# Kernel optimization log

Measured on AMD Instinct MI355X. Metric: run time of the kernel, lower is better.

## Reference

```python
import jax, jax.numpy as jnp
import numpy as np

N, L, H, DH = 4, 1024, 16, 64
D = H * DH  # 1024
DFF = 4 * D
NEG_INF = jnp.float32(-1e30)  # used via actual -inf per torch masked_fill


def layer_norm(x, g, b, eps=1e-5):
    mu = jnp.mean(x, axis=-1, keepdims=True)
    var = jnp.mean(jnp.square(x - mu), axis=-1, keepdims=True)
    return (x - mu) * jax.lax.rsqrt(var + eps) * g + b


def mha(q_in, k_in, Wq, Wk, Wv, mask, padding_mask):
    # q_in: (N,Lq,D), k_in: (N,Lk,D); Linear weights (D,D), out = x @ W.T
    n, Lq, _ = q_in.shape
    Lk = k_in.shape[1]
    q = jnp.einsum('nld,od->nlo', q_in, Wq).reshape(n, Lq, H, DH)
    k = jnp.einsum('nld,od->nlo', k_in, Wk).reshape(n, Lk, H, DH)
    v = jnp.einsum('nld,od->nlo', k_in, Wv).reshape(n, Lk, H, DH)
    # per-sample scaling = sqrt(#non-padded keys)
    scaling = jnp.sqrt(jnp.sum(~padding_mask, axis=-1).astype(q.dtype))  # (N,)
    score = jnp.einsum('nqhd,nkhd->nhqk', q, k) / scaling[:, None, None, None]
    if mask is not None:
        score = jnp.where(mask[None, None, :, :], -jnp.inf, score)
    score = jnp.where(padding_mask[:, None, None, :], -jnp.inf, score)
    p = jax.nn.softmax(score, axis=-1)
    out = jnp.einsum('nhqk,nkhd->nqhd', p, v).reshape(n, Lq, D)
    return out


def setup_inputs() -> dict:
    key = jax.random.key(0)
    ks = jax.random.split(key, 16)
    s = 0.02
    inp = {
        'encoded': jax.random.normal(ks[0], (N, L, D), jnp.float32),
        'Y': jax.random.normal(ks[1], (N, L, D), jnp.float32),
        # causal mask: True above diagonal -> attention set to -inf
        'mask': ~jnp.tril(jnp.ones((L, L), dtype=bool)),
        # suffix padding with varied per-sample lengths (all >= 1)
        'padding_mask': jnp.arange(L)[None, :] >= jnp.array([L, 3 * L // 4, L // 2, 7 * L // 8])[:, None],
        # masked self-attention projections
        'Wq1': jax.random.normal(ks[2], (D, D), jnp.float32) * s,
        'Wk1': jax.random.normal(ks[3], (D, D), jnp.float32) * s,
        'Wv1': jax.random.normal(ks[4], (D, D), jnp.float32) * s,
        'g1': jnp.ones((D,), jnp.float32), 'b1': jnp.zeros((D,), jnp.float32),
        # cross-attention projections
        'Wq2': jax.random.normal(ks[5], (D, D), jnp.float32) * s,
        'Wk2': jax.random.normal(ks[6], (D, D), jnp.float32) * s,
        'Wv2': jax.random.normal(ks[7], (D, D), jnp.float32) * s,
        'g2': jnp.ones((D,), jnp.float32), 'b2': jnp.zeros((D,), jnp.float32),
        # FFN
        'We': jax.random.normal(ks[8], (DFF, D), jnp.float32) * s,
        'be': jnp.zeros((DFF,), jnp.float32),
        'Wc': jax.random.normal(ks[9], (D, DFF), jnp.float32) * s,
        'bc': jnp.zeros((D,), jnp.float32),
        'g3': jnp.ones((D,), jnp.float32), 'b3': jnp.zeros((D,), jnp.float32),
    }
    return inp


def reference(encoded, Y, mask, padding_mask,
              Wq1, Wk1, Wv1, g1, b1,
              Wq2, Wk2, Wv2, g2, b2,
              We, be, Wc, bc, g3, b3):
    # masked self-attention + residual + LN (dropout=0 -> identity)
    res = Y
    a = mha(Y, Y, Wq1, Wk1, Wv1, mask, padding_mask)
    Y = layer_norm(a + res, g1, b1)
    # cross-attention (no causal mask) + residual + LN
    res = Y
    a = mha(Y, encoded, Wq2, Wk2, Wv2, None, padding_mask)
    Y = layer_norm(a + res, g2, b2)
    # FFN + residual + LN
    res = Y
    h = jax.nn.relu(jnp.einsum('nld,fd->nlf', Y, We) + be)
    h = jnp.einsum('nlf,df->nld', h, Wc) + bc
    Y = layer_norm(h + res, g3, b3)
    return Y
```

## Files before the change

### kernel.cpp

```cpp
#include <hip/hip_runtime.h>
#include <stdint.h>

#define NB 4
#define LS 1024
#define HH 16
#define DHD 64
#define DM 1024
#define DF 4096
#define QKS 2048

typedef unsigned short u16;
typedef __attribute__((ext_vector_type(4))) float f32x4;
typedef __attribute__((ext_vector_type(8))) __bf16 bf16x8;
typedef __attribute__((ext_vector_type(8))) unsigned short u16x8;

__device__ __forceinline__ u16 f2bf(float f) {
  union { float f; uint32_t u; } v; v.f = f;
  uint32_t u = v.u;
  return (u16)((u + 0x7fffu + ((u >> 16) & 1u)) >> 16);
}

__device__ __forceinline__ bf16x8 ldb8(const u16* p) {
  u16x8 r = *(const u16x8*)p;
  return __builtin_bit_cast(bf16x8, r);
}

__device__ __forceinline__ void gload_lds16(const u16* g, u16* l) {
  __builtin_amdgcn_global_load_lds((const __attribute__((address_space(1))) void*)g,
                                   (__attribute__((address_space(3))) void*)l,
                                   16, 0, 0);
}

#define WAITV10() asm volatile("s_waitcnt vmcnt(10)" ::: "memory")
#define BARRIER()                      \
  do {                                 \
    asm volatile("" ::: "memory");     \
    __builtin_amdgcn_s_barrier();      \
    asm volatile("" ::: "memory");     \
  } while (0)

__global__ void prep_kernel(const uint32_t* __restrict__ pm, int* lens, float* iscl) {
  __shared__ int flagByte;
  __shared__ int red[256];
  int tid = threadIdx.x;
  if (tid == 0) flagByte = 0;
  __syncthreads();
  int f = 0;
  for (int w = tid; w < (NB * LS) / 4; w += 256) {
    uint32_t u = pm[w];
    if (u != 0u && u != 1u && u != 0x3f800000u) f = 1;
  }
  if (f) atomicOr(&flagByte, 1);
  __syncthreads();
  int isByte = flagByte;
  for (int n = 0; n < NB; n++) {
    int c = 0;
    if (isByte) {
      const uint8_t* pb = (const uint8_t*)pm;
      for (int l = tid; l < LS; l += 256) c += (pb[n * LS + l] == 0) ? 1 : 0;
    } else {
      for (int l = tid; l < LS; l += 256) c += (pm[n * LS + l] == 0) ? 1 : 0;
    }
    red[tid] = c;
    __syncthreads();
    for (int s = 128; s > 0; s >>= 1) {
      if (tid < s) red[tid] += red[tid + s];
      __syncthreads();
    }
    if (tid == 0) { lens[n] = red[0]; iscl[n] = 1.0f / sqrtf((float)red[0]); }
    __syncthreads();
  }
}

__global__ void cvt_all(const float* s0, u16* d0, const float* s1, u16* d1,
                        const float* s2, u16* d2, const float* s3, u16* d3,
                        const float* s4, u16* d4, const float* s5, u16* d5,
                        const float* s6, u16* d6, const float* s7, u16* d7,
                        const float* s8, u16* d8, const float* s9, u16* d9) {
  const int total = 5767168;
  int i = blockIdx.x * 256 + threadIdx.x;
  for (; i < total; i += gridDim.x * 256) {
    const float* s; u16* d; int j;
    if (i < 1048576)      { s = s0; d = d0; j = i; }
    else if (i < 2097152) { s = s1; d = d1; j = i - 1048576; }
    else if (i < 2359296) { s = s2; d = d2; j = i - 2097152; }
    else if (i < 2621440) { s = s3; d = d3; j = i - 2359296; }
    else if (i < 2883584) { s = s4; d = d4; j = i - 2621440; }
    else if (i < 3145728) { s = s5; d = d5; j = i - 2883584; }
    else if (i < 3407872) { s = s6; d = d6; j = i - 3145728; }
    else if (i < 3670016) { s = s7; d = d7; j = i - 3407872; }
    else if (i < 4718592) { s = s8; d = d8; j = i - 3670016; }
    else                  { s = s9; d = d9; j = i - 4718592; }
    float4 fv = ((const float4*)s)[j];
    ushort4 o;
    o.x = f2bf(fv.x); o.y = f2bf(fv.y); o.z = f2bf(fv.z); o.w = f2bf(fv.w);
    ((ushort4*)d)[j] = o;
  }
}

template <int MODE>
__global__ __launch_bounds__(512, 2) void gemm8(
    const u16* __restrict__ P0, const u16* __restrict__ P1,
    const u16* __restrict__ PW, const float* __restrict__ bias,
    void* __restrict__ O0, void* __restrict__ O1,
    void* __restrict__ O2, void* __restrict__ O3) {
  extern __shared__ u16 lds[];
  constexpr int NT = 16;
  const int bm = blockIdx.x;
  const int tid = threadIdx.x;
  const int wid = tid >> 6, lane = tid & 63;
  const int lrow = lane & 15, lgrp = lane >> 4;
  const int wm = wid >> 2, wn = wid & 3;

  const u16* Asrc; const u16* Bsrc; int lda, ldb;
  if constexpr (MODE == 0) {
    Asrc = P0 + (size_t)bm * 256 * DM; lda = DM;
    Bsrc = PW + (size_t)blockIdx.y * 256 * DM; ldb = DM;
  } else if constexpr (MODE == 1) {
    const int z = blockIdx.z;
    Asrc = P0 + (size_t)bm * 256 * DF + z * 1024; lda = DF;
    Bsrc = PW + (size_t)blockIdx.y * 256 * DF + z * 1024; ldb = DF;
  } else {
    const int bnt = blockIdx.y;
    Asrc = (bnt < 12 ? P0 : P1) + (size_t)bm * 256 * DM; lda = DM;
    const int wrow = (bnt < 12) ? bnt * 256 : 4096 + (bnt - 12) * 256;
    Bsrc = PW + (size_t)wrow * DM; ldb = DM;
  }

  int srow[2], skk[2];
#pragma unroll
  for (int i = 0; i < 2; i++) {
    const int c = (i * 8 + wid) * 64 + lane;
    const int pair = c >> 3;
    const int ue = ((c & 7) * 8) ^ ((pair & 7) << 3);
    srow[i] = pair * 2 + (ue >> 5);
    skk[i] = ue & 31;
  }
  const int dslot0 = wid * 512;
  const int dslot1 = (8 + wid) * 512;

  f32x4 acc[2][4][4] = {};

  auto STAGE_A = [&](int kt, int buf, int kh) {
    const int ks = kt < NT ? kt : NT - 1;
    gload_lds16(Asrc + (size_t)srow[0] * lda + ks * 64 + kh * 32 + skk[0],
                lds + buf * 16384 + kh * 8192 + dslot0);
    gload_lds16(Asrc + (size_t)srow[1] * lda + ks * 64 + kh * 32 + skk[1],
                lds + buf * 16384 + kh * 8192 + dslot1);
  };
  auto STAGE_B = [&](int kt, int buf, int kh) {
    const int ks = kt < NT ? kt : NT - 1;
    gload_lds16(Bsrc + (size_t)srow[0] * ldb + ks * 64 + kh * 32 + skk[0],
                lds + 32768 + buf * 16384 + kh * 8192 + dslot0);
    gload_lds16(Bsrc + (size_t)srow[1] * ldb + ks * 64 + kh * 32 + skk[1],
                lds + 32768 + buf * 16384 + kh * 8192 + dslot1);
  };
  auto LDA = [&](int buf, int kh, int mh, bf16x8* a) {
#pragma unroll
    for (int m = 0; m < 4; m++) {
      const int row = wm * 128 + mh * 64 + m * 16 + lrow;
      const int idx = buf * 16384 + kh * 8192 + (row >> 1) * 64 +
                      ((((row & 1) << 5) + (lgrp << 3)) ^ (((row >> 1) & 7) << 3));
      a[m] = ldb8(lds + idx);
    }
  };
  auto LDB = [&](int buf, int kh, bf16x8* b) {
#pragma unroll
    for (int nn = 0; nn < 4; nn++) {
      const int row = wn * 64 + nn * 16 + lrow;
      const int idx = 32768 + buf * 16384 + kh * 8192 + (row >> 1) * 64 +
                      ((((row & 1) << 5) + (lgrp << 3)) ^ (((row >> 1) & 7) << 3));
      b[nn] = ldb8(lds + idx);
    }
  };

  STAGE_A(0, 0, 0); STAGE_B(0, 0, 0);
  STAGE_A(0, 0, 1); STAGE_B(0, 0, 1);
  STAGE_A(1, 1, 0); STAGE_B(1, 1, 0);

  for (int t = 0; t < NT; t++) {
    const int b = t & 1;
    bf16x8 af[4], bf[4];
    STAGE_A(t + 1, b ^ 1, 1);
    WAITV10();
    BARRIER();
    LDA(b, 0, 0, af); LDB(b, 0, bf);
    __builtin_amdgcn_s_setprio(1);
#pragma unroll
    for (int m = 0; m < 4; m++)
#pragma unroll
      for (int nn = 0; nn < 4; nn++)
        acc[0][m][nn] = __builtin_amdgcn_mfma_f32_16x16x32_bf16(af[m], bf[nn], acc[0][m][nn], 0, 0, 0);
    __builtin_amdgcn_s_setprio(0);
    STAGE_B(t + 1, b ^ 1, 1);
    LDA(b, 0, 1, af);
    __builtin_amdgcn_s_setprio(1);
#pragma unroll
    for (int m = 0; m < 4; m++)
#pragma unroll
      for (int nn = 0; nn < 4; nn++)
        acc[1][m][nn] = __builtin_amdgcn_mfma_f32_16x16x32_bf16(af[m], bf[nn], acc[1][m][nn], 0, 0, 0);
    __builtin_amdgcn_s_setprio(0);
    BARRIER();
    STAGE_A(t + 2, b, 0);
    WAITV10();
    BARRIER();
    LDA(b, 1, 0, af); LDB(b, 1, bf);
    __builtin_amdgcn_s_setprio(1);
#pragma unroll
    for (int m = 0; m < 4; m++)
#pragma unroll
      for (int nn = 0; nn < 4; nn++)
        acc[0][m][nn] = __builtin_amdgcn_mfma_f32_16x16x32_bf16(af[m], bf[nn], acc[0][m][nn], 0, 0, 0);
    __builtin_amdgcn_s_setprio(0);
    STAGE_B(t + 2, b, 0);
    LDA(b, 1, 1, af);
    __builtin_amdgcn_s_setprio(1);
#pragma unroll
    for (int m = 0; m < 4; m++)
#pragma unroll
      for (int nn = 0; nn < 4; nn++)
        acc[1][m][nn] = __builtin_amdgcn_mfma_f32_16x16x32_bf16(af[m], bf[nn], acc[1][m][nn], 0, 0, 0);
    __builtin_amdgcn_s_setprio(0);
    BARRIER();
  }

#pragma unroll
  for (int mh = 0; mh < 2; mh++)
#pragma unroll
    for (int m = 0; m < 4; m++) {
      const int grow0 = bm * 256 + wm * 128 + mh * 64 + m * 16 + lgrp * 4;
#pragma unroll
      for (int nn = 0; nn < 4; nn++) {
        const int col_l = wn * 64 + nn * 16 + lrow;
        f32x4 v = acc[mh][m][nn];
        if constexpr (MODE == 0) {
          const int col = blockIdx.y * 256 + col_l;
          const float bv = bias[col];
#pragma unroll
          for (int r = 0; r < 4; r++) {
            float x = v[r] + bv;
            x = x > 0.0f ? x : 0.0f;
            ((u16*)O0)[(size_t)(grow0 + r) * DF + col] = f2bf(x);
          }
        } else if constexpr (MODE == 1) {
          float* C = (float*)O0 + (size_t)blockIdx.z * ((size_t)NB * LS * DM);
          const int col = blockIdx.y * 256 + col_l;
#pragma unroll
          for (int r = 0; r < 4; r++) C[(size_t)(grow0 + r) * DM + col] = v[r];
        } else {
          const int bnt = blockIdx.y;
          const int nidx = grow0 >> 10, l0 = grow0 & 1023;
          if (bnt < 8) {
            const int col = bnt * 256 + col_l;
#pragma unroll
            for (int r = 0; r < 4; r++)
              ((u16*)O0)[(size_t)(grow0 + r) * QKS + col] = f2bf(v[r]);
          } else if (bnt < 12) {
            const int vc = (bnt - 8) * 256 + col_l;
            ushort4 o;
            o.x = f2bf(v[0]); o.y = f2bf(v[1]); o.z = f2bf(v[2]); o.w = f2bf(v[3]);
            *(ushort4*)((u16*)O1 + (((size_t)(nidx * HH + (vc >> 6)) * DHD + (vc & 63)) << 10) + l0) = o;
          } else if (bnt < 16) {
            const int col = 1024 + (bnt - 12) * 256 + col_l;
#pragma unroll
            for (int r = 0; r < 4; r++)
              ((u16*)O2)[(size_t)(grow0 + r) * QKS + col] = f2bf(v[r]);
          } else {
            const int vc = (bnt - 16) * 256 + col_l;
            ushort4 o;
            o.x = f2bf(v[0]); o.y = f2bf(v[1]); o.z = f2bf(v[2]); o.w = f2bf(v[3]);
            *(ushort4*)((u16*)O3 + (((size_t)(nidx * HH + (vc >> 6)) * DHD + (vc & 63)) << 10) + l0) = o;
          }
        }
      }
    }
}

template <int EPI>
__global__ __launch_bounds__(256) void gemm_bt(const u16* __restrict__ A, int lda,
                                               const u16* __restrict__ B, int ldb,
                                               const float* __restrict__ bias,
                                               void* __restrict__ Cout, int ldc,
                                               int Klen, size_t zcstride) {
  __shared__ u16 Al[128 * 32];
  __shared__ u16 Bl[128 * 32];
  const int tid = threadIdx.x;
  const int bm = blockIdx.x, bn = blockIdx.y, z = blockIdx.z;
  const int wave = tid >> 6, lane = tid & 63;
  const int lrow = lane & 15, lgrp = lane >> 4;
  const int wr = (wave >> 1) * 64, wc = (wave & 1) * 64;
  f32x4 acc[4][4] = {};
  const u16* Ab = A + (size_t)bm * 128 * lda + (size_t)z * Klen;
  const u16* Bb = B + (size_t)bn * 128 * ldb + (size_t)z * Klen;
  char* Cz = (char*)Cout + (size_t)z * zcstride;
  {
    const int c0 = wave, c1 = wave + 4;
    const int r0 = c0 * 16 + (lane >> 2), r1 = c1 * 16 + (lane >> 2);
    const int scc = (lane & 3) * 8;
    const u16* Ag0 = Ab + (size_t)r0 * lda + scc;
    const u16* Ag1 = Ab + (size_t)r1 * lda + scc;
    const u16* Bg0 = Bb + (size_t)r0 * ldb + scc;
    const u16* Bg1 = Bb + (size_t)r1 * ldb + scc;
    u16* Ad0 = Al + c0 * 512;
    u16* Ad1 = Al + c1 * 512;
    u16* Bd0 = Bl + c0 * 512;
    u16* Bd1 = Bl + c1 * 512;
    for (int kb = 0; kb < Klen; kb += 32) {
      gload_lds16(Ag0, Ad0);
      gload_lds16(Ag1, Ad1);
      gload_lds16(Bg0, Bd0);
      gload_lds16(Bg1, Bd1);
      Ag0 += 32; Ag1 += 32; Bg0 += 32; Bg1 += 32;
      __syncthreads();
      bf16x8 af[4], bfr[4];
#pragma unroll
      for (int m = 0; m < 4; m++) af[m] = ldb8(Al + (wr + m * 16 + lrow) * 32 + lgrp * 8);
#pragma unroll
      for (int nn = 0; nn < 4; nn++) bfr[nn] = ldb8(Bl + (wc + nn * 16 + lrow) * 32 + lgrp * 8);
#pragma unroll
      for (int m = 0; m < 4; m++)
#pragma unroll
        for (int nn = 0; nn < 4; nn++)
          acc[m][nn] = __builtin_amdgcn_mfma_f32_16x16x32_bf16(af[m], bfr[nn], acc[m][nn], 0, 0, 0);
      __syncthreads();
    }
  }
#pragma unroll
  for (int m = 0; m < 4; m++) {
    const int row0 = bm * 128 + wr + m * 16 + lgrp * 4;
#pragma unroll
    for (int nn = 0; nn < 4; nn++) {
      const int col = bn * 128 + wc + nn * 16 + lrow;
      float bv = (EPI == 1) ? bias[col] : 0.0f;
#pragma unroll
      for (int r = 0; r < 4; r++) {
        float v = acc[m][nn][r];
        if (EPI == 1) { v += bv; v = v > 0.0f ? v : 0.0f; }
        size_t idx = (size_t)(row0 + r) * ldc + col;
        if (EPI == 4) ((float*)Cz)[idx] = v;
        else ((u16*)Cz)[idx] = f2bf(v);
      }
    }
  }
}

template <bool CAUSAL>
__global__ __launch_bounds__(256) void attn_kernel(const u16* __restrict__ QK,
                                                   const u16* __restrict__ Vt,
                                                   float* __restrict__ Out,
                                                   const int* __restrict__ lens,
                                                   const float* __restrict__ iscl) {
  __shared__ u16 Kl[64 * 72];
  __shared__ u16 Vl[64 * 72];
  __shared__ u16 Pl[4][16 * 72];
  const int n = blockIdx.z, h = blockIdx.y, qb = blockIdx.x * 64;
  const int tid = threadIdx.x, wave = tid >> 6, lane = tid & 63;
  const int lrow = lane & 15, lgrp = lane >> 4;
  const int len = lens[n];
  const float isc = iscl[n];
  const int qrow = qb + wave * 16 + lrow;
  const u16* qptr = QK + ((size_t)(n * LS + qrow)) * QKS + h * DHD + lgrp * 8;
  bf16x8 qf0 = ldb8(qptr);
  bf16x8 qf1 = ldb8(qptr + 32);
  f32x4 oacc[4] = {};
  float m_run[4], l_run[4];
#pragma unroll
  for (int r = 0; r < 4; r++) { m_run[r] = -1e30f; l_run[r] = 0.0f; }
  const int kend = CAUSAL ? (len < qb + 64 ? len : qb + 64) : len;
  const int srow = tid >> 3, sc = (tid & 7) * 8;
  const u16* kg_base = QK + 1024 + ((size_t)(n * LS)) * QKS + h * DHD + sc;
  const u16* vg_base = Vt + ((size_t)((n * HH + h) * DHD) + srow) * LS + sc;
  u16* pw = Pl[wave];
  for (int kb = 0; kb < kend; kb += 64) {
    __syncthreads();
#pragma unroll
    for (int i = 0; i < 2; i++) {
      const int row = srow + i * 32;
      u16x8 kv = *(const u16x8*)(kg_base + (size_t)(kb + row) * QKS);
      *(u16x8*)(Kl + row * 72 + sc) = kv;
      u16x8 vv = *(const u16x8*)(vg_base + (size_t)(i * 32) * LS + kb);
      *(u16x8*)(Vl + row * 72 + sc) = vv;
    }
    __syncthreads();
    f32x4 s[4];
#pragma unroll
    for (int st = 0; st < 4; st++) {
      const u16* kr = Kl + (st * 16 + lrow) * 72 + lgrp * 8;
      bf16x8 kf0 = ldb8(kr);
      bf16x8 kf1 = ldb8(kr + 32);
      f32x4 z = {};
      z = __builtin_amdgcn_mfma_f32_16x16x32_bf16(qf0, kf0, z, 0, 0, 0);
      s[st] = __builtin_amdgcn_mfma_f32_16x16x32_bf16(qf1, kf1, z, 0, 0, 0);
    }
    const int q_r = qb + wave * 16 + lgrp * 4;
#pragma unroll
    for (int st = 0; st < 4; st++) {
      const int k = kb + st * 16 + lrow;
#pragma unroll
      for (int r = 0; r < 4; r++) {
        float v = s[st][r] * isc;
        bool ok = (k < len) && (!CAUSAL || k <= q_r + r);
        s[st][r] = ok ? v : -1e30f;
      }
    }
#pragma unroll
    for (int r = 0; r < 4; r++) {
      float mx = fmaxf(fmaxf(s[0][r], s[1][r]), fmaxf(s[2][r], s[3][r]));
      mx = fmaxf(mx, __shfl_xor(mx, 1));
      mx = fmaxf(mx, __shfl_xor(mx, 2));
      mx = fmaxf(mx, __shfl_xor(mx, 4));
      mx = fmaxf(mx, __shfl_xor(mx, 8));
      float mn = fmaxf(m_run[r], mx);
      float fac = __expf(m_run[r] - mn);
      m_run[r] = mn;
      float sm = 0.0f;
#pragma unroll
      for (int st = 0; st < 4; st++) {
        float p = __expf(s[st][r] - mn);
        s[st][r] = p;
        sm += p;
      }
      sm += __shfl_xor(sm, 1);
      sm += __shfl_xor(sm, 2);
      sm += __shfl_xor(sm, 4);
      sm += __shfl_xor(sm, 8);
      l_run[r] = l_run[r] * fac + sm;
#pragma unroll
      for (int dt = 0; dt < 4; dt++) oacc[dt][r] *= fac;
    }
#pragma unroll
    for (int st = 0; st < 4; st++)
#pragma unroll
      for (int r = 0; r < 4; r++)
        pw[(lgrp * 4 + r) * 72 + st * 16 + lrow] = f2bf(s[st][r]);
#pragma unroll
    for (int ks = 0; ks < 2; ks++) {
      bf16x8 pf = ldb8(pw + lrow * 72 + ks * 32 + lgrp * 8);
#pragma unroll
      for (int dt = 0; dt < 4; dt++) {
        bf16x8 vf = ldb8(Vl + (dt * 16 + lrow) * 72 + ks * 32 + lgrp * 8);
        oacc[dt] = __builtin_amdgcn_mfma_f32_16x16x32_bf16(pf, vf, oacc[dt], 0, 0, 0);
      }
    }
  }
#pragma unroll
  for (int r = 0; r < 4; r++) {
    float inv = 1.0f / l_run[r];
    const int row = qb + wave * 16 + lgrp * 4 + r;
    float* op = Out + ((size_t)(n * LS + row)) * DM + h * DHD;
#pragma unroll
    for (int dt = 0; dt < 4; dt++) op[dt * 16 + lrow] = oacc[dt][r] * inv;
  }
}

__global__ __launch_bounds__(256) void ln_kernel(const float* __restrict__ a,
                                                 const float* __restrict__ res,
                                                 const float* __restrict__ g,
                                                 const float* __restrict__ bta,
                                                 float* __restrict__ outf,
                                                 u16* __restrict__ outb) {
  const int row = blockIdx.x, tid = threadIdx.x;
  float4 x = ((const float4*)(a + (size_t)row * DM))[tid];
  float4 rr = ((const float4*)(res + (size_t)row * DM))[tid];
  x.x += rr.x; x.y += rr.y; x.z += rr.z; x.w += rr.w;
  float s = x.x + x.y + x.z + x.w;
  float s2 = x.x * x.x + x.y * x.y + x.z * x.z + x.w * x.w;
#pragma unroll
  for (int m = 1; m < 64; m <<= 1) { s += __shfl_xor(s, m); s2 += __shfl_xor(s2, m); }
  __shared__ float sm[8];
  const int wv = tid >> 6;
  if ((tid & 63) == 0) { sm[wv] = s; sm[4 + wv] = s2; }
  __syncthreads();
  s = sm[0] + sm[1] + sm[2] + sm[3];
  s2 = sm[4] + sm[5] + sm[6] + sm[7];
  const float mean = s * (1.0f / (float)DM);
  const float var = s2 * (1.0f / (float)DM) - mean * mean;
  const float inv = rsqrtf(var + 1e-5f);
  float4 gg = ((const float4*)g)[tid];
  float4 bb = ((const float4*)bta)[tid];
  float4 y;
  y.x = (x.x - mean) * inv * gg.x + bb.x;
  y.y = (x.y - mean) * inv * gg.y + bb.y;
  y.z = (x.z - mean) * inv * gg.z + bb.z;
  y.w = (x.w - mean) * inv * gg.w + bb.w;
  ((float4*)(outf + (size_t)row * DM))[tid] = y;
  if (outb) {
    ushort4 o;
    o.x = f2bf(y.x); o.y = f2bf(y.y); o.z = f2bf(y.z); o.w = f2bf(y.w);
    ((ushort4*)(outb + (size_t)row * DM))[tid] = o;
  }
}

__global__ __launch_bounds__(256) void ln_final(const float* __restrict__ part,
                                                const float* __restrict__ bias,
                                                const float* __restrict__ res,
                                                const float* __restrict__ g,
                                                const float* __restrict__ bta,
                                                float* __restrict__ outf) {
  const int row = blockIdx.x, tid = threadIdx.x;
  const size_t PS = (size_t)NB * LS * DM;
  float4 x = ((const float4*)(part + (size_t)row * DM))[tid];
  float4 p1 = ((const float4*)(part + PS + (size_t)row * DM))[tid];
  float4 p2 = ((const float4*)(part + 2 * PS + (size_t)row * DM))[tid];
  float4 p3 = ((const float4*)(part + 3 * PS + (size_t)row * DM))[tid];
  float4 bb4 = ((const float4*)bias)[tid];
  float4 rr = ((const float4*)(res + (size_t)row * DM))[tid];
  x.x += p1.x + p2.x + p3.x + bb4.x + rr.x;
  x.y += p1.y + p2.y + p3.y + bb4.y + rr.y;
  x.z += p1.z + p2.z + p3.z + bb4.z + rr.z;
  x.w += p1.w + p2.w + p3.w + bb4.w + rr.w;
  float s = x.x + x.y + x.z + x.w;
  float s2 = x.x * x.x + x.y * x.y + x.z * x.z + x.w * x.w;
#pragma unroll
  for (int m = 1; m < 64; m <<= 1) { s += __shfl_xor(s, m); s2 += __shfl_xor(s2, m); }
  __shared__ float sm[8];
  const int wv = tid >> 6;
  if ((tid & 63) == 0) { sm[wv] = s; sm[4 + wv] = s2; }
  __syncthreads();
  s = sm[0] + sm[1] + sm[2] + sm[3];
  s2 = sm[4] + sm[5] + sm[6] + sm[7];
  const float mean = s * (1.0f / (float)DM);
  const float var = s2 * (1.0f / (float)DM) - mean * mean;
  const float inv = rsqrtf(var + 1e-5f);
  float4 gg = ((const float4*)g)[tid];
  float4 bb = ((const float4*)bta)[tid];
  float4 y;
  y.x = (x.x - mean) * inv * gg.x + bb.x;
  y.y = (x.y - mean) * inv * gg.y + bb.y;
  y.z = (x.z - mean) * inv * gg.z + bb.z;
  y.w = (x.w - mean) * inv * gg.w + bb.w;
  ((float4*)(outf + (size_t)row * DM))[tid] = y;
}

extern "C" void kernel_launch(void* const* d_in, const int* in_sizes, int n_in,
                              void* d_out, int out_size, void* d_ws, size_t ws_size,
                              hipStream_t stream) {
  const float* enc = (const float*)d_in[0];
  const float* Yin = (const float*)d_in[1];
  const uint32_t* pmask = (const uint32_t*)d_in[3];
  const float* Wq1 = (const float*)d_in[4];
  const float* Wk1 = (const float*)d_in[5];
  const float* Wv1 = (const float*)d_in[6];
  const float* g1 = (const float*)d_in[7];
  const float* b1 = (const float*)d_in[8];
  const float* Wq2 = (const float*)d_in[9];
  const float* Wk2 = (const float*)d_in[10];
  const float* Wv2 = (const float*)d_in[11];
  const float* g2 = (const float*)d_in[12];
  const float* b2 = (const float*)d_in[13];
  const float* We = (const float*)d_in[14];
  const float* be = (const float*)d_in[15];
  const float* Wc = (const float*)d_in[16];
  const float* bc = (const float*)d_in[17];
  const float* g3 = (const float*)d_in[18];
  const float* b3 = (const float*)d_in[19];

  const size_t ACT = (size_t)NB * LS * DM;
  const size_t WSZ = (size_t)DM * DM;
  const size_t WFF = (size_t)DF * DM;
  const size_t HID = (size_t)NB * LS * DF;

  char* ws = (char*)d_ws;
  size_t off = 0;
  auto alloc = [&](size_t bytes) -> void* {
    void* p = ws + off;
    off += (bytes + 255) & ~(size_t)255;
    return p;
  };
  int* lens = (int*)alloc(64);
  float* iscl = (float*)alloc(64);
  u16* Ybf = (u16*)alloc(ACT * 2);
  u16* Ebf = (u16*)alloc(ACT * 2);
  u16* W6 = (u16*)alloc(WSZ * 6 * 2);
  u16* Web = (u16*)alloc(WFF * 2);
  u16* Wcb = (u16*)alloc(WFF * 2);
  size_t region0 = off;
  u16* QKa = (u16*)alloc((size_t)NB * LS * QKS * 2);
  u16* VtA = (u16*)alloc(ACT * 2);
  u16* QKb = (u16*)alloc((size_t)NB * LS * QKS * 2);
  u16* VtB = (u16*)alloc(ACT * 2);
  float* aout = (float*)alloc(ACT * 4);
  float* y2 = (float*)alloc(ACT * 4);
  float* part = (float*)(ws + region0);
  float* y3 = (float*)alloc(ACT * 4);
  u16* Hb = (u16*)alloc(HID * 2);

  prep_kernel<<<1, 256, 0, stream>>>(pmask, lens, iscl);
  cvt_all<<<2048, 256, 0, stream>>>(Yin, Ybf, enc, Ebf,
                                    Wq1, W6 + 0 * WSZ, Wk1, W6 + 1 * WSZ,
                                    Wv1, W6 + 2 * WSZ, Wq2, W6 + 3 * WSZ,
                                    Wk2, W6 + 4 * WSZ, Wv2, W6 + 5 * WSZ,
                                    We, Web, Wc, Wcb);

  dim3 blk(256);
  gemm8<2><<<dim3(16, 20), 512, 131072, stream>>>(Ybf, Ebf, W6, nullptr,
                                                  QKa, VtA, QKb, VtB);
  attn_kernel<true><<<dim3(16, 16, 4), blk, 0, stream>>>(QKa, VtA, aout, lens, iscl);
  ln_kernel<<<NB * LS, 256, 0, stream>>>(aout, Yin, g1, b1, y2, Ybf);
  gemm_bt<0><<<dim3(32, 8), blk, 0, stream>>>(Ybf, DM, W6 + 3 * WSZ, DM, nullptr,
                                              QKb, QKS, DM, 0);
  attn_kernel<false><<<dim3(16, 16, 4), blk, 0, stream>>>(QKb, VtB, aout, lens, iscl);
  ln_kernel<<<NB * LS, 256, 0, stream>>>(aout, y2, g2, b2, y3, Ebf);
  gemm8<0><<<dim3(16, 16), 512, 131072, stream>>>(Ebf, nullptr, Web, be,
                                                  Hb, nullptr, nullptr, nullptr);
  gemm8<1><<<dim3(16, 4, 4), 512, 131072, stream>>>(Hb, nullptr, Wcb, nullptr,
                                                    part, nullptr, nullptr, nullptr);
  ln_final<<<NB * LS, 256, 0, stream>>>(part, bc, y3, g3, b3, (float*)d_out);
}
```

Baseline: 347.3 us.

## Restructure GEMM main loop to issue LDS reads before global stages and barriers

Reorders the 256x256 GEMM inner loop so each phase loads the A/B fragments from LDS first, then issues the next global-to-LDS stage, and runs the MFMA block between barriers. The waitcnt moves from vmcnt(10) to vmcnt(8), and a prologue wait plus barrier and a final vmcnt(0) drain are added. The aim is to overlap LDS reads and global loads with MFMA work in a more regular ping-pong schedule. It adds extra barriers per iteration, which may cost synchronisation time, and changes the buffer hazard ordering.

```diff
diff --git a/kernel.cpp b/kernel.cpp
--- a/kernel.cpp
+++ b/kernel.cpp
@@ -31,7 +31,8 @@
                                    16, 0, 0);
 }
 
-#define WAITV10() asm volatile("s_waitcnt vmcnt(10)" ::: "memory")
+#define WAITV8() asm volatile("s_waitcnt vmcnt(8)" ::: "memory")
+#define WAITV0() asm volatile("s_waitcnt vmcnt(0)" ::: "memory")
 #define BARRIER()                      \
   do {                                 \
     asm volatile("" ::: "memory");     \
@@ -173,57 +174,49 @@
       b[nn] = ldb8(lds + idx);
     }
   };
+  auto MFMA16 = [&](f32x4 (&a4)[4][4], bf16x8* af, bf16x8* bk) {
+    __builtin_amdgcn_s_setprio(1);
+#pragma unroll
+    for (int m = 0; m < 4; m++)
+#pragma unroll
+      for (int nn = 0; nn < 4; nn++)
+        a4[m][nn] = __builtin_amdgcn_mfma_f32_16x16x32_bf16(af[m], bk[nn], a4[m][nn], 0, 0, 0);
+    __builtin_amdgcn_s_setprio(0);
+  };
 
   STAGE_A(0, 0, 0); STAGE_B(0, 0, 0);
   STAGE_A(0, 0, 1); STAGE_B(0, 0, 1);
   STAGE_A(1, 1, 0); STAGE_B(1, 1, 0);
+  WAITV8();
+  BARRIER();
 
   for (int t = 0; t < NT; t++) {
     const int b = t & 1;
-    bf16x8 af[4], bf[4];
+    bf16x8 af[4], bk[4];
+    LDA(b, 0, 0, af); LDB(b, 0, bk);
     STAGE_A(t + 1, b ^ 1, 1);
-    WAITV10();
-    BARRIER();
-    LDA(b, 0, 0, af); LDB(b, 0, bf);
-    __builtin_amdgcn_s_setprio(1);
-#pragma unroll
-    for (int m = 0; m < 4; m++)
-#pragma unroll
-      for (int nn = 0; nn < 4; nn++)
-        acc[0][m][nn] = __builtin_amdgcn_mfma_f32_16x16x32_bf16(af[m], bf[nn], acc[0][m][nn], 0, 0, 0);
-    __builtin_amdgcn_s_setprio(0);
+    BARRIER();
+    MFMA16(acc[0], af, bk);
+    BARRIER();
+    LDA(b, 0, 1, af);
     STAGE_B(t + 1, b ^ 1, 1);
-    LDA(b, 0, 1, af);
-    __builtin_amdgcn_s_setprio(1);
-#pragma unroll
-    for (int m = 0; m < 4; m++)
-#pragma unroll
-      for (int nn = 0; nn < 4; nn++)
-        acc[1][m][nn] = __builtin_amdgcn_mfma_f32_16x16x32_bf16(af[m], bf[nn], acc[1][m][nn], 0, 0, 0);
-    __builtin_amdgcn_s_setprio(0);
-    BARRIER();
+    WAITV8();
+    BARRIER();
+    MFMA16(acc[1], af, bk);
+    BARRIER();
+    LDA(b, 1, 0, af); LDB(b, 1, bk);
     STAGE_A(t + 2, b, 0);
-    WAITV10();
-    BARRIER();
-    LDA(b, 1, 0, af); LDB(b, 1, bf);
-    __builtin_amdgcn_s_setprio(1);
-#pragma unroll
-    for (int m = 0; m < 4; m++)
-#pragma unroll
-      for (int nn = 0; nn < 4; nn++)
-        acc[0][m][nn] = __builtin_amdgcn_mfma_f32_16x16x32_bf16(af[m], bf[nn], acc[0][m][nn], 0, 0, 0);
-    __builtin_amdgcn_s_setprio(0);
+    BARRIER();
+    MFMA16(acc[0], af, bk);
+    BARRIER();
+    LDA(b, 1, 1, af);
     STAGE_B(t + 2, b, 0);
-    LDA(b, 1, 1, af);
-    __builtin_amdgcn_s_setprio(1);
-#pragma unroll
-    for (int m = 0; m < 4; m++)
-#pragma unroll
-      for (int nn = 0; nn < 4; nn++)
-        acc[1][m][nn] = __builtin_amdgcn_mfma_f32_16x16x32_bf16(af[m], bf[nn], acc[1][m][nn], 0, 0, 0);
-    __builtin_amdgcn_s_setprio(0);
-    BARRIER();
-  }
+    WAITV8();
+    BARRIER();
+    MFMA16(acc[1], af, bk);
+    BARRIER();
+  }
+  WAITV0();
 
 #pragma unroll
   for (int mh = 0; mh < 2; mh++)
```

Measured after the change: 349.1 us. No clear change (+0.5%).
